# Performance work log

Hardware: AMD Instinct MI355X
Metric: run time of the kernel (lower is better)

Reference implementation:

```python
import jax, jax.numpy as jnp
import numpy as np

B, C_IN, T = 32, 192, 8192
H, N_PH, OUT = 192, 1024, 4
EPS = 1e-5


def setup_inputs() -> dict:
    key = jax.random.key(0)
    ks = jax.random.split(key, 12)
    s = 0.02
    return {
        "x": jax.random.normal(ks[0], (B, C_IN, T), jnp.float32),
        "x_mask": jnp.ones((B, 1, N_PH), jnp.float32),
        "w": jax.random.randint(ks[1], (B, 1, N_PH), 0, 8, jnp.int32),
        "pre_w": jax.random.normal(ks[2], (H, C_IN), jnp.float32) * s,
        "pre_b": jnp.zeros((H,), jnp.float32),
        "conv0_w": jax.random.normal(ks[3], (H, H, 3), jnp.float32) * s,
        "conv0_b": jnp.zeros((H,), jnp.float32),
        "ln0_g": jnp.ones((H,), jnp.float32),
        "ln0_b": jnp.zeros((H,), jnp.float32),
        "conv1_w": jax.random.normal(ks[4], (H, H, 3), jnp.float32) * s,
        "conv1_b": jnp.zeros((H,), jnp.float32),
        "ln1_g": jnp.ones((H,), jnp.float32),
        "ln1_b": jnp.zeros((H,), jnp.float32),
        "lin_w": jax.random.normal(ks[5], (OUT, H), jnp.float32) * s,
        "lin_b": jnp.zeros((OUT,), jnp.float32),
    }


def _segment_mean(x, w2):
    # x: [B, C, T] frames; w2: [B, n_ph] int durations.
    # Faithful to the torch double loop: phoneme j pools frames
    # [cumsum(w)[j-1] : cumsum(w)[j]); w==0 -> zeros.
    ends = jnp.cumsum(w2, axis=1)                      # [B, n_ph]
    t = jnp.arange(x.shape[2], dtype=ends.dtype)       # [T]
    ph_id = jax.vmap(lambda e: jnp.searchsorted(e, t, side="right"))(ends)  # [B, T]
    # segment sums over frames; extra segment n_ph catches out-of-range frames
    sums = jax.vmap(lambda xt, ids: jax.ops.segment_sum(xt, ids, num_segments=N_PH + 1))(
        x.transpose(0, 2, 1), ph_id
    )                                                  # [B, n_ph+1, C]
    sums = sums[:, :N_PH].transpose(0, 2, 1)           # [B, C, n_ph]
    denom = jnp.maximum(w2, 1).astype(x.dtype)[:, None, :]
    return jnp.where(w2[:, None, :] > 0, sums / denom, 0.0)


def _conv3(x, k, b):
    y = jax.lax.conv_general_dilated(x, k, (1,), [(1, 1)],
                                     dimension_numbers=("NCH", "OIH", "NCH"))
    return y + b[None, :, None]


def _ln(x, g, b):
    # channel-dim LayerNorm for [B, C, T] (VITS modules.LayerNorm)
    m = jnp.mean(x, axis=1, keepdims=True)
    v = jnp.mean(jnp.square(x - m), axis=1, keepdims=True)
    return (x - m) * jax.lax.rsqrt(v + EPS) * g[None, :, None] + b[None, :, None]


def reference(x, x_mask, w, pre_w, pre_b, conv0_w, conv0_b, ln0_g, ln0_b,
              conv1_w, conv1_b, ln1_g, ln1_b, lin_w, lin_b):
    w2 = w.reshape(w.shape[0], -1).astype(jnp.int32)
    spec = _segment_mean(x, w2)                                 # [B, C_in, n_ph]
    h = jnp.einsum("bct,hc->bht", spec, pre_w) + pre_b[None, :, None]
    # block 0: conv -> relu -> LN (dropout is identity at eval), mask before each layer
    h = _conv3(h * x_mask, conv0_w, conv0_b)
    h = jax.nn.relu(h * x_mask)
    h = _ln(h * x_mask, ln0_g, ln0_b)
    h = h * x_mask  # dropout(p=0.1) at eval = identity; mask still applied
    # block 1
    h = _conv3(h * x_mask, conv1_w, conv1_b)
    h = jax.nn.relu(h * x_mask)
    h = _ln(h * x_mask, ln1_g, ln1_b)
    h = h * x_mask
    p = jnp.einsum("bht,oh->bot", h, lin_w) + lin_b[None, :, None]
    return p * x_mask
```

## Files before the change

kernel.cpp:

```cpp
#include <hip/hip_runtime.h>
#include <hip/hip_bf16.h>

#define B 32
#define C_IN 192
#define T 8192
#define H 192
#define N_PH 1024
#define OUT 4
#define PROWS (N_PH + 2)
#define ROWP (2 * H)

typedef __attribute__((ext_vector_type(8))) short short8;
typedef __attribute__((ext_vector_type(4))) float f32x4;
typedef unsigned short ushort_t;

__device__ inline ushort_t f2bf(float f) {
    unsigned u = __builtin_bit_cast(unsigned, f);
    unsigned r = u + 0x7fffu + ((u >> 16) & 1u);
    return (ushort_t)(r >> 16);
}
__device__ inline float bf2f(ushort_t h) {
    unsigned u = ((unsigned)h) << 16;
    return __builtin_bit_cast(float, u);
}
__device__ inline void split_bf(float x, ushort_t& hi, ushort_t& lo) {
    hi = f2bf(x);
    lo = f2bf(x - bf2f(hi));
}

__device__ inline void wfrag_one(const float* __restrict__ w, ushort_t* __restrict__ wtf,
                                 int taps, int idx, int ntot) {
    int j  = idx & 7;
    int l  = (idx >> 3) & 63;
    int slot = idx >> 9;
    int nt = slot % 12;
    int ss = (slot / 12) % 6;
    int kt = slot / 72;
    int o  = nt * 16 + (l & 15);
    int i  = ss * 32 + ((l >> 4) << 3) + j;
    float v = (taps == 1) ? w[o * C_IN + i] : w[(o * H + i) * 3 + kt];
    ushort_t hi, lo;
    split_bf(v, hi, lo);
    wtf[idx] = hi;
    wtf[idx + ntot] = lo;
}

#define NWF 1008
__global__ __launch_bounds__(256) void prep_kernel(
    const float* __restrict__ pw, const float* __restrict__ w0,
    const float* __restrict__ w1, const int* __restrict__ wdur,
    ushort_t* __restrict__ wpre, ushort_t* __restrict__ w0t,
    ushort_t* __restrict__ w1t, int* __restrict__ ends)
{
    int blk = blockIdx.x;
    int tid = threadIdx.x;
    const int n1 = 36864, n3 = 110592;
    if (blk < NWF) {
        int idx = blk * 256 + tid;
        if (idx < n1) { wfrag_one(pw, wpre, 1, idx, n1); return; }
        idx -= n1;
        if (idx < n3) { wfrag_one(w0, w0t, 3, idx, n3); return; }
        idx -= n3;
        if (idx < n3) wfrag_one(w1, w1t, 3, idx, n3);
        return;
    }
    int b = blk - NWF;
    __shared__ int part[256];
    int4 w4 = ((const int4*)(wdur + b * N_PH))[tid];
    int c0 = w4.x, c1 = c0 + w4.y, c2 = c1 + w4.z, c3 = c2 + w4.w;
    part[tid] = c3;
    __syncthreads();
    for (int off = 1; off < 256; off <<= 1) {
        int v = (tid >= off) ? part[tid - off] : 0;
        __syncthreads();
        part[tid] += v;
        __syncthreads();
    }
    int pre = tid ? part[tid - 1] : 0;
    int4 e4;
    e4.x = pre + c0; e4.y = pre + c1; e4.z = pre + c2; e4.w = pre + c3;
    ((int4*)(ends + b * N_PH))[tid] = e4;
}

__global__ __launch_bounds__(256) void segmean_direct_kernel(
    const float* __restrict__ x, const int* __restrict__ ends,
    ushort_t* __restrict__ specT)
{
    int b  = blockIdx.x >> 5;
    int jt = (blockIdx.x & 31) * 32;
    int tid = threadIdx.x;
    int j_loc = tid & 31;
    int cg0 = tid >> 5;
    int j = jt + j_loc;

    __shared__ float sm[32][193];

    const int* eb = ends + b * N_PH;
    int e0 = eb[j];
    int s0 = j ? eb[j - 1] : 0;
    int len = e0 - s0;
    float inv = (len > 0) ? 1.f / (float)len : 0.f;

    const float* xb = x + (size_t)b * C_IN * T;
#pragma unroll 1
    for (int c = cg0; c < C_IN; c += 8) {
        const float* xr = xb + (size_t)c * T;
        float sum = 0.f;
        for (int t = s0; t < e0; ++t) sum += xr[t];
        sm[j_loc][c] = sum * inv;
    }
    __syncthreads();

    int r = tid >> 3;
    int g = tid & 7;
    ushort_t* ob = specT + ((size_t)b * N_PH + jt + r) * ROWP;
#pragma unroll
    for (int i0 = 0; i0 < 24; i0 += 8) {
        ushort_t th[8], tl[8];
#pragma unroll
        for (int k2 = 0; k2 < 8; ++k2) {
            int c = g * 24 + i0 + k2;
            split_bf(sm[r][c], th[k2], tl[k2]);
        }
        *(short8*)(ob + g * 24 + i0) = *(short8*)th;
        *(short8*)(ob + H + g * 24 + i0) = *(short8*)tl;
    }
}

#define LOADOPS(IT, AH0, AL0, AH1, AL1, BH, BL) do {                              \
    int kt_ = (IT) / 6, s_ = (IT) - kt_ * 6;                                      \
    const ushort_t* arow_ = inb + (long)(trow + kt_ - pad) * ROWP + s_ * 32 + kg; \
    AH0 = *(const short8*)(arow_);                                                \
    AL0 = *(const short8*)(arow_ + H);                                            \
    AH1 = *(const short8*)(arow_ + 16 * ROWP);                                    \
    AL1 = *(const short8*)(arow_ + 16 * ROWP + H);                                \
    const ushort_t* wb_ = wt + ((size_t)((kt_ * 6 + s_) * 12 + nhalf * 6) << 9)   \
                        + (lane << 3);                                            \
    _Pragma("unroll") for (int n_ = 0; n_ < 6; ++n_) {                            \
        BH[n_] = *(const short8*)(wb_ + (n_ << 9));                               \
        BL[n_] = *(const short8*)(wb_ + (n_ << 9) + ntotw); }                     \
} while (0)

#define DOMFMA(AH0, AL0, AH1, AL1, BH, BL) do {                                             \
    _Pragma("unroll") for (int n_ = 0; n_ < 6; ++n_) {                                      \
        acc[0][n_] = __builtin_amdgcn_mfma_f32_16x16x32_bf16(AH0, BH[n_], acc[0][n_], 0,0,0); \
        acc[0][n_] = __builtin_amdgcn_mfma_f32_16x16x32_bf16(AL0, BH[n_], acc[0][n_], 0,0,0); \
        acc[0][n_] = __builtin_amdgcn_mfma_f32_16x16x32_bf16(AH0, BL[n_], acc[0][n_], 0,0,0); \
        acc[1][n_] = __builtin_amdgcn_mfma_f32_16x16x32_bf16(AH1, BH[n_], acc[1][n_], 0,0,0); \
        acc[1][n_] = __builtin_amdgcn_mfma_f32_16x16x32_bf16(AL1, BH[n_], acc[1][n_], 0,0,0); \
        acc[1][n_] = __builtin_amdgcn_mfma_f32_16x16x32_bf16(AH1, BL[n_], acc[1][n_], 0,0,0); } \
} while (0)

__global__ __launch_bounds__(256) void gemm_fused_kernel(
    const ushort_t* __restrict__ in, int in_rows,
    const ushort_t* __restrict__ wt,
    const float* __restrict__ bias,
    const float* __restrict__ mask,
    const float* __restrict__ g, const float* __restrict__ beta,
    ushort_t* __restrict__ out,
    const float* __restrict__ lw, const float* __restrict__ lb,
    float* __restrict__ fout,
    int taps, int do_ln, int nmask, int fin)
{
    int b  = blockIdx.y;
    int t0 = blockIdx.x * 64;
    int tid = threadIdx.x;
    int lane = tid & 63;
    int wv = tid >> 6;
    int mhalf = wv & 1;
    int nhalf = wv >> 1;

    __shared__ float ep[64][193];
    __shared__ float g_s[H], b_s[H], m_s[64], mstat[64], rstat[64];
    if (tid < H) { g_s[tid] = do_ln ? g[tid] : 1.f; b_s[tid] = do_ln ? beta[tid] : 0.f; }
    if (tid < 64) m_s[tid] = mask[b * N_PH + t0 + tid];

    short8 z8 = {0, 0, 0, 0, 0, 0, 0, 0};
    if (!fin) {
        if (t0 == 0 && tid < ROWP / 8)
            *(short8*)(out + (size_t)b * PROWS * ROWP + tid * 8) = z8;
        if (t0 == N_PH - 64 && tid < ROWP / 8)
            *(short8*)(out + ((size_t)b * PROWS + N_PH + 1) * ROWP + tid * 8) = z8;
    }

    int m  = lane & 15;
    int kg = (lane >> 4) << 3;
    int ntotw = taps * 36864;
    int pad = taps >> 1;

    const ushort_t* inb = in + (size_t)b * in_rows * ROWP;
    int trow = t0 + mhalf * 32 + m;

    f32x4 acc[2][6];
#pragma unroll
    for (int ntl = 0; ntl < 6; ++ntl) {
        float bb = bias[(nhalf * 6 + ntl) * 16 + m];
        acc[0][ntl] = (f32x4){bb, bb, bb, bb};
        acc[1][ntl] = (f32x4){bb, bb, bb, bb};
    }

    short8 pah0, pal0, pah1, pal1, pbh[6], pbl[6];
    short8 qah0, qal0, qah1, qal1, qbh[6], qbl[6];
    int iters = taps * 6;
    LOADOPS(0, pah0, pal0, pah1, pal1, pbh, pbl);
#pragma unroll 1
    for (int it = 0; it < iters; it += 2) {
        LOADOPS(it + 1, qah0, qal0, qah1, qal1, qbh, qbl);
        DOMFMA(pah0, pal0, pah1, pal1, pbh, pbl);
        if (it + 2 < iters) LOADOPS(it + 2, pah0, pal0, pah1, pal1, pbh, pbl);
        DOMFMA(qah0, qal0, qah1, qal1, qbh, qbl);
    }

    __syncthreads();

    int rbase = (lane >> 4) << 2;
#pragma unroll
    for (int mh = 0; mh < 2; ++mh) {
#pragma unroll
        for (int ntl = 0; ntl < 6; ++ntl) {
            int o = (nhalf * 6 + ntl) * 16 + m;
#pragma unroll
            for (int r = 0; r < 4; ++r) {
                int t_loc = mhalf * 32 + mh * 16 + rbase + r;
                float mm = m_s[t_loc];
                float v = acc[mh][ntl][r];
                if (do_ln) {
                    v = fmaxf(v * mm, 0.f) * mm;
                } else {
                    for (int q = 0; q < nmask; ++q) v *= mm;
                }
                ep[t_loc][o] = v;
            }
        }
    }
    __syncthreads();

    if (do_ln && tid < 64) {
        float s = 0.f, ss = 0.f;
        for (int c = 0; c < H; ++c) {
            float v = ep[tid][c];
            s += v;
            ss += v * v;
        }
        float mean = s * (1.f / (float)H);
        mstat[tid] = mean;
        rstat[tid] = rsqrtf(ss * (1.f / (float)H) - mean * mean + 1e-5f);
    }
    __syncthreads();

    int row = tid >> 2;
    int q = tid & 3;
    if (fin) {
        float mean = mstat[row], rstd = rstat[row], mk = m_s[row];
        float a0 = 0.f, a1 = 0.f, a2 = 0.f, a3 = 0.f;
#pragma unroll 1
        for (int c = q * 48; c < q * 48 + 48; ++c) {
            float y = ((ep[row][c] - mean) * rstd * g_s[c] + b_s[c]) * mk;
            a0 += lw[0 * H + c] * y;
            a1 += lw[1 * H + c] * y;
            a2 += lw[2 * H + c] * y;
            a3 += lw[3 * H + c] * y;
        }
        a0 += __shfl_xor(a0, 1); a0 += __shfl_xor(a0, 2);
        a1 += __shfl_xor(a1, 1); a1 += __shfl_xor(a1, 2);
        a2 += __shfl_xor(a2, 1); a2 += __shfl_xor(a2, 2);
        a3 += __shfl_xor(a3, 1); a3 += __shfl_xor(a3, 2);
        if (q == 0) {
            int t = t0 + row;
            float* ob = fout + (size_t)b * OUT * N_PH + t;
            ob[0 * N_PH] = (a0 + lb[0]) * mk;
            ob[1 * N_PH] = (a1 + lb[1]) * mk;
            ob[2 * N_PH] = (a2 + lb[2]) * mk;
            ob[3 * N_PH] = (a3 + lb[3]) * mk;
        }
        return;
    }

    float mean = 0.f, rstd = 1.f, mfac = 1.f;
    if (do_ln) {
        mean = mstat[row];
        rstd = rstat[row];
        float mk = m_s[row];
        mfac = (nmask == 2) ? mk * mk : mk;
    }
    ushort_t* orow = out + ((size_t)b * PROWS + t0 + row + 1) * ROWP + q * 48;
#pragma unroll
    for (int i0 = 0; i0 < 48; i0 += 8) {
        ushort_t th[8], tl[8];
#pragma unroll
        for (int k2 = 0; k2 < 8; ++k2) {
            int c = q * 48 + i0 + k2;
            float v = ep[row][c];
            float y = do_ln ? ((v - mean) * rstd * g_s[c] + b_s[c]) * mfac : v;
            split_bf(y, th[k2], tl[k2]);
        }
        *(short8*)(orow + i0) = *(short8*)th;
        *(short8*)(orow + H + i0) = *(short8*)tl;
    }
}

extern "C" void kernel_launch(void* const* d_in, const int* in_sizes, int n_in,
                              void* d_out, int out_size, void* d_ws, size_t ws_size,
                              hipStream_t stream) {
    const float* x      = (const float*)d_in[0];
    const float* x_mask = (const float*)d_in[1];
    const int*   w      = (const int*)d_in[2];
    const float* pre_w  = (const float*)d_in[3];
    const float* pre_b  = (const float*)d_in[4];
    const float* conv0_w = (const float*)d_in[5];
    const float* conv0_b = (const float*)d_in[6];
    const float* ln0_g   = (const float*)d_in[7];
    const float* ln0_b   = (const float*)d_in[8];
    const float* conv1_w = (const float*)d_in[9];
    const float* conv1_b = (const float*)d_in[10];
    const float* ln1_g   = (const float*)d_in[11];
    const float* ln1_b   = (const float*)d_in[12];
    const float* lin_w   = (const float*)d_in[13];
    const float* lin_b   = (const float*)d_in[14];
    float* out = (float*)d_out;

    char* ws = (char*)d_ws;
    size_t off = 0;
    ushort_t* bufA = (ushort_t*)(ws + off); off += (size_t)B * PROWS * ROWP * sizeof(ushort_t);
    ushort_t* bufB = (ushort_t*)(ws + off); off += (size_t)B * PROWS * ROWP * sizeof(ushort_t);
    ushort_t* wpre = (ushort_t*)(ws + off); off += (size_t)2 * 36864 * sizeof(ushort_t);
    ushort_t* w0t  = (ushort_t*)(ws + off); off += (size_t)2 * 110592 * sizeof(ushort_t);
    ushort_t* w1t  = (ushort_t*)(ws + off); off += (size_t)2 * 110592 * sizeof(ushort_t);
    int* ends      = (int*)(ws + off);      off += (size_t)B * N_PH * sizeof(int);
    ushort_t* specT = bufB;

    prep_kernel<<<NWF + B, 256, 0, stream>>>(pre_w, conv0_w, conv1_w, w,
                                             wpre, w0t, w1t, ends);

    segmean_direct_kernel<<<B * 32, 256, 0, stream>>>(x, ends, specT);

    dim3 gg(N_PH / 64, B);
    gemm_fused_kernel<<<gg, 256, 0, stream>>>(specT, N_PH, wpre, pre_b, x_mask,
                                              ln0_g, ln0_b, bufA,
                                              nullptr, nullptr, nullptr, 1, 0, 1, 0);
    gemm_fused_kernel<<<gg, 256, 0, stream>>>(bufA + ROWP, PROWS, w0t, conv0_b, x_mask,
                                              ln0_g, ln0_b, bufB,
                                              nullptr, nullptr, nullptr, 3, 1, 2, 0);
    gemm_fused_kernel<<<gg, 256, 0, stream>>>(bufB + ROWP, PROWS, w1t, conv1_b, x_mask,
                                              ln1_g, ln1_b, bufA,
                                              lin_w, lin_b, out, 3, 1, 1, 1);
}
```

Before: 401.8 us.

## Fuse pre-projection, both conv blocks and output linear into one halo-tiled kernel

```diff
diff --git a/kernel.cpp b/kernel.cpp
--- a/kernel.cpp
+++ b/kernel.cpp
@@ -7,8 +7,8 @@
 #define H 192
 #define N_PH 1024
 #define OUT 4
-#define PROWS (N_PH + 2)
 #define ROWP (2 * H)
+#define HPITCH 392
 
 typedef __attribute__((ext_vector_type(8))) short short8;
 typedef __attribute__((ext_vector_type(4))) float f32x4;
@@ -127,139 +127,273 @@
     }
 }
 
-#define LOADOPS(IT, AH0, AL0, AH1, AL1, BH, BL) do {                              \
-    int kt_ = (IT) / 6, s_ = (IT) - kt_ * 6;                                      \
-    const ushort_t* arow_ = inb + (long)(trow + kt_ - pad) * ROWP + s_ * 32 + kg; \
-    AH0 = *(const short8*)(arow_);                                                \
-    AL0 = *(const short8*)(arow_ + H);                                            \
-    AH1 = *(const short8*)(arow_ + 16 * ROWP);                                    \
-    AL1 = *(const short8*)(arow_ + 16 * ROWP + H);                                \
-    const ushort_t* wb_ = wt + ((size_t)((kt_ * 6 + s_) * 12 + nhalf * 6) << 9)   \
-                        + (lane << 3);                                            \
-    _Pragma("unroll") for (int n_ = 0; n_ < 6; ++n_) {                            \
-        BH[n_] = *(const short8*)(wb_ + (n_ << 9));                               \
-        BL[n_] = *(const short8*)(wb_ + (n_ << 9) + ntotw); }                     \
-} while (0)
-
-#define DOMFMA(AH0, AL0, AH1, AL1, BH, BL) do {                                             \
-    _Pragma("unroll") for (int n_ = 0; n_ < 6; ++n_) {                                      \
-        acc[0][n_] = __builtin_amdgcn_mfma_f32_16x16x32_bf16(AH0, BH[n_], acc[0][n_], 0,0,0); \
-        acc[0][n_] = __builtin_amdgcn_mfma_f32_16x16x32_bf16(AL0, BH[n_], acc[0][n_], 0,0,0); \
-        acc[0][n_] = __builtin_amdgcn_mfma_f32_16x16x32_bf16(AH0, BL[n_], acc[0][n_], 0,0,0); \
-        acc[1][n_] = __builtin_amdgcn_mfma_f32_16x16x32_bf16(AH1, BH[n_], acc[1][n_], 0,0,0); \
-        acc[1][n_] = __builtin_amdgcn_mfma_f32_16x16x32_bf16(AL1, BH[n_], acc[1][n_], 0,0,0); \
-        acc[1][n_] = __builtin_amdgcn_mfma_f32_16x16x32_bf16(AH1, BL[n_], acc[1][n_], 0,0,0); } \
-} while (0)
-
-__global__ __launch_bounds__(256) void gemm_fused_kernel(
-    const ushort_t* __restrict__ in, int in_rows,
-    const ushort_t* __restrict__ wt,
-    const float* __restrict__ bias,
+__global__ __launch_bounds__(256) void chain_kernel(
+    const ushort_t* __restrict__ specT,
+    const ushort_t* __restrict__ wpre, const ushort_t* __restrict__ w0t,
+    const ushort_t* __restrict__ w1t,
+    const float* __restrict__ pre_b, const float* __restrict__ c0_b,
+    const float* __restrict__ c1_b,
     const float* __restrict__ mask,
-    const float* __restrict__ g, const float* __restrict__ beta,
-    ushort_t* __restrict__ out,
+    const float* __restrict__ g0, const float* __restrict__ be0,
+    const float* __restrict__ g1, const float* __restrict__ be1,
     const float* __restrict__ lw, const float* __restrict__ lb,
-    float* __restrict__ fout,
-    int taps, int do_ln, int nmask, int fin)
+    float* __restrict__ out)
 {
-    int b  = blockIdx.y;
-    int t0 = blockIdx.x * 64;
-    int tid = threadIdx.x;
-    int lane = tid & 63;
-    int wv = tid >> 6;
-    int mhalf = wv & 1;
-    int nhalf = wv >> 1;
-
-    __shared__ float ep[64][193];
-    __shared__ float g_s[H], b_s[H], m_s[64], mstat[64], rstat[64];
-    if (tid < H) { g_s[tid] = do_ln ? g[tid] : 1.f; b_s[tid] = do_ln ? beta[tid] : 0.f; }
-    if (tid < 64) m_s[tid] = mask[b * N_PH + t0 + tid];
-
-    short8 z8 = {0, 0, 0, 0, 0, 0, 0, 0};
-    if (!fin) {
-        if (t0 == 0 && tid < ROWP / 8)
-            *(short8*)(out + (size_t)b * PROWS * ROWP + tid * 8) = z8;
-        if (t0 == N_PH - 64 && tid < ROWP / 8)
-            *(short8*)(out + ((size_t)b * PROWS + N_PH + 1) * ROWP + tid * 8) = z8;
-    }
-
-    int m  = lane & 15;
-    int kg = (lane >> 4) << 3;
-    int ntotw = taps * 36864;
-    int pad = taps >> 1;
-
-    const ushort_t* inb = in + (size_t)b * in_rows * ROWP;
-    int trow = t0 + mhalf * 32 + m;
-
-    f32x4 acc[2][6];
-#pragma unroll
-    for (int ntl = 0; ntl < 6; ++ntl) {
-        float bb = bias[(nhalf * 6 + ntl) * 16 + m];
-        acc[0][ntl] = (f32x4){bb, bb, bb, bb};
-        acc[1][ntl] = (f32x4){bb, bb, bb, bb};
-    }
-
-    short8 pah0, pal0, pah1, pal1, pbh[6], pbl[6];
-    short8 qah0, qal0, qah1, qal1, qbh[6], qbl[6];
-    int iters = taps * 6;
-    LOADOPS(0, pah0, pal0, pah1, pal1, pbh, pbl);
-#pragma unroll 1
-    for (int it = 0; it < iters; it += 2) {
-        LOADOPS(it + 1, qah0, qal0, qah1, qal1, qbh, qbl);
-        DOMFMA(pah0, pal0, pah1, pal1, pbh, pbl);
-        if (it + 2 < iters) LOADOPS(it + 2, pah0, pal0, pah1, pal1, pbh, pbl);
-        DOMFMA(qah0, qal0, qah1, qal1, qbh, qbl);
-    }
-
-    __syncthreads();
-
-    int rbase = (lane >> 4) << 2;
-#pragma unroll
-    for (int mh = 0; mh < 2; ++mh) {
-#pragma unroll
-        for (int ntl = 0; ntl < 6; ++ntl) {
-            int o = (nhalf * 6 + ntl) * 16 + m;
-#pragma unroll
-            for (int r = 0; r < 4; ++r) {
-                int t_loc = mhalf * 32 + mh * 16 + rbase + r;
-                float mm = m_s[t_loc];
-                float v = acc[mh][ntl][r];
-                if (do_ln) {
-                    v = fmaxf(v * mm, 0.f) * mm;
-                } else {
-                    for (int q = 0; q < nmask; ++q) v *= mm;
-                }
-                ep[t_loc][o] = v;
-            }
-        }
-    }
-    __syncthreads();
-
-    if (do_ln && tid < 64) {
+    const int b  = blockIdx.y;
+    const int t0 = blockIdx.x * 64;
+    const int tid = threadIdx.x;
+    const int lane = tid & 63;
+    const int wv = tid >> 6;
+    const int nhalf = wv >> 1;
+    const int mgrp = wv & 1;
+    const int m = lane & 15;
+    const int kg = (lane >> 4) << 3;
+    const int rbase = (lane >> 4) << 2;
+
+    __shared__ ushort_t hbuf[82 * HPITCH];
+    __shared__ float g0_s[H], b0_s[H], g1_s[H], b1_s[H];
+    __shared__ float lw_s[OUT * H];
+    __shared__ float m_s[96], mstat[66], rstat[66];
+
+    if (tid < H) { g0_s[tid] = g0[tid]; b0_s[tid] = be0[tid];
+                   g1_s[tid] = g1[tid]; b1_s[tid] = be1[tid]; }
+    if (tid < 96) {
+        int grow = t0 - 2 + tid;
+        m_s[tid] = (grow >= 0 && grow < N_PH) ? mask[b * N_PH + grow] : 0.f;
+    }
+    for (int i = tid; i < OUT * H; i += 256) lw_s[i] = lw[i];
+    __syncthreads();
+
+    const short8 z8 = {0, 0, 0, 0, 0, 0, 0, 0};
+
+    {
+        f32x4 acc[3][6];
+#pragma unroll
+        for (int n = 0; n < 6; ++n) {
+            float bb = pre_b[(nhalf * 6 + n) * 16 + m];
+#pragma unroll
+            for (int f = 0; f < 3; ++f) acc[f][n] = (f32x4){bb, bb, bb, bb};
+        }
+        const ushort_t* inb = specT + (size_t)b * N_PH * ROWP;
+#pragma unroll 1
+        for (int s = 0; s < 6; ++s) {
+            short8 ah[3], al[3], bh[6], bl[6];
+#pragma unroll
+            for (int f = 0; f < 3; ++f) {
+                int trow = t0 - 2 + (mgrp * 3 + f) * 16 + m;
+                if ((unsigned)trow < (unsigned)N_PH) {
+                    const ushort_t* ar = inb + (size_t)trow * ROWP + s * 32 + kg;
+                    ah[f] = *(const short8*)ar;
+                    al[f] = *(const short8*)(ar + H);
+                } else { ah[f] = z8; al[f] = z8; }
+            }
+            const ushort_t* wb = wpre + ((size_t)(s * 12 + nhalf * 6) << 9) + (lane << 3);
+#pragma unroll
+            for (int n = 0; n < 6; ++n) {
+                bh[n] = *(const short8*)(wb + (n << 9));
+                bl[n] = *(const short8*)(wb + (n << 9) + 36864);
+            }
+#pragma unroll
+            for (int f = 0; f < 3; ++f)
+#pragma unroll
+                for (int n = 0; n < 6; ++n) {
+                    acc[f][n] = __builtin_amdgcn_mfma_f32_16x16x32_bf16(ah[f], bh[n], acc[f][n], 0, 0, 0);
+                    acc[f][n] = __builtin_amdgcn_mfma_f32_16x16x32_bf16(al[f], bh[n], acc[f][n], 0, 0, 0);
+                    acc[f][n] = __builtin_amdgcn_mfma_f32_16x16x32_bf16(ah[f], bl[n], acc[f][n], 0, 0, 0);
+                }
+        }
+#pragma unroll
+        for (int f = 0; f < 3; ++f) {
+            int lb0 = (mgrp * 3 + f) * 16 + rbase;
+#pragma unroll
+            for (int n = 0; n < 6; ++n) {
+                int col = (nhalf * 6 + n) * 16 + m;
+#pragma unroll
+                for (int r = 0; r < 4; ++r) {
+                    int l = lb0 + r;
+                    if (l < 82) {
+                        float v = acc[f][n][r] * m_s[l];
+                        ushort_t hi, lo; split_bf(v, hi, lo);
+                        hbuf[l * HPITCH + col] = hi;
+                        hbuf[l * HPITCH + H + col] = lo;
+                    }
+                }
+            }
+        }
+    }
+    __syncthreads();
+
+    {
+        f32x4 acc[3][6];
+        const int nf = mgrp ? 2 : 3;
+        const int fbase = mgrp * 3;
+#pragma unroll
+        for (int n = 0; n < 6; ++n) {
+            float bb = c0_b[(nhalf * 6 + n) * 16 + m];
+#pragma unroll
+            for (int f = 0; f < 3; ++f) acc[f][n] = (f32x4){bb, bb, bb, bb};
+        }
+#pragma unroll 1
+        for (int kt = 0; kt < 3; ++kt)
+#pragma unroll 1
+            for (int s = 0; s < 6; ++s) {
+                short8 ah[3], al[3], bh[6], bl[6];
+#pragma unroll
+                for (int f = 0; f < 3; ++f) {
+                    if (f < nf) {
+                        int l0 = (fbase + f) * 16 + m + kt;
+                        const ushort_t* ar = hbuf + l0 * HPITCH + s * 32 + kg;
+                        ah[f] = *(const short8*)ar;
+                        al[f] = *(const short8*)(ar + H);
+                    }
+                }
+                const ushort_t* wb = w0t + ((size_t)((kt * 6 + s) * 12 + nhalf * 6) << 9) + (lane << 3);
+#pragma unroll
+                for (int n = 0; n < 6; ++n) {
+                    bh[n] = *(const short8*)(wb + (n << 9));
+                    bl[n] = *(const short8*)(wb + (n << 9) + 110592);
+                }
+#pragma unroll
+                for (int f = 0; f < 3; ++f) {
+                    if (f < nf) {
+#pragma unroll
+                        for (int n = 0; n < 6; ++n) {
+                            acc[f][n] = __builtin_amdgcn_mfma_f32_16x16x32_bf16(ah[f], bh[n], acc[f][n], 0, 0, 0);
+                            acc[f][n] = __builtin_amdgcn_mfma_f32_16x16x32_bf16(al[f], bh[n], acc[f][n], 0, 0, 0);
+                            acc[f][n] = __builtin_amdgcn_mfma_f32_16x16x32_bf16(ah[f], bl[n], acc[f][n], 0, 0, 0);
+                        }
+                    }
+                }
+            }
+        __syncthreads();
+#pragma unroll
+        for (int f = 0; f < 3; ++f) {
+            if (f < nf) {
+                int lb1 = (fbase + f) * 16 + rbase;
+#pragma unroll
+                for (int n = 0; n < 6; ++n) {
+                    int col = (nhalf * 6 + n) * 16 + m;
+#pragma unroll
+                    for (int r = 0; r < 4; ++r) {
+                        int l = lb1 + r;
+                        if (l < 66) {
+                            float mm = m_s[l + 1];
+                            float u = fmaxf(acc[f][n][r] * mm, 0.f) * mm;
+                            ushort_t hi, lo; split_bf(u, hi, lo);
+                            hbuf[l * HPITCH + col] = hi;
+                            hbuf[l * HPITCH + H + col] = lo;
+                        }
+                    }
+                }
+            }
+        }
+    }
+    __syncthreads();
+
+    if (tid < 66) {
         float s = 0.f, ss = 0.f;
         for (int c = 0; c < H; ++c) {
-            float v = ep[tid][c];
-            s += v;
-            ss += v * v;
+            float v = bf2f(hbuf[tid * HPITCH + c]) + bf2f(hbuf[tid * HPITCH + H + c]);
+            s += v; ss += v * v;
         }
         float mean = s * (1.f / (float)H);
         mstat[tid] = mean;
         rstat[tid] = rsqrtf(ss * (1.f / (float)H) - mean * mean + 1e-5f);
     }
     __syncthreads();
-
-    int row = tid >> 2;
-    int q = tid & 3;
-    if (fin) {
-        float mean = mstat[row], rstd = rstat[row], mk = m_s[row];
+    for (int idx = tid; idx < 66 * H; idx += 256) {
+        int row = idx / H;
+        int c = idx - row * H;
+        float v = bf2f(hbuf[row * HPITCH + c]) + bf2f(hbuf[row * HPITCH + H + c]);
+        float mm = m_s[row + 1];
+        float y = ((v - mstat[row]) * rstat[row] * g0_s[c] + b0_s[c]) * (mm * mm);
+        ushort_t hi, lo; split_bf(y, hi, lo);
+        hbuf[row * HPITCH + c] = hi;
+        hbuf[row * HPITCH + H + c] = lo;
+    }
+    __syncthreads();
+
+    {
+        f32x4 acc[2][6];
+#pragma unroll
+        for (int n = 0; n < 6; ++n) {
+            float bb = c1_b[(nhalf * 6 + n) * 16 + m];
+            acc[0][n] = (f32x4){bb, bb, bb, bb};
+            acc[1][n] = (f32x4){bb, bb, bb, bb};
+        }
+#pragma unroll 1
+        for (int kt = 0; kt < 3; ++kt)
+#pragma unroll 1
+            for (int s = 0; s < 6; ++s) {
+                short8 ah[2], al[2], bh[6], bl[6];
+#pragma unroll
+                for (int f = 0; f < 2; ++f) {
+                    int l1 = (mgrp * 2 + f) * 16 + m + kt;
+                    const ushort_t* ar = hbuf + l1 * HPITCH + s * 32 + kg;
+                    ah[f] = *(const short8*)ar;
+                    al[f] = *(const short8*)(ar + H);
+                }
+                const ushort_t* wb = w1t + ((size_t)((kt * 6 + s) * 12 + nhalf * 6) << 9) + (lane << 3);
+#pragma unroll
+                for (int n = 0; n < 6; ++n) {
+                    bh[n] = *(const short8*)(wb + (n << 9));
+                    bl[n] = *(const short8*)(wb + (n << 9) + 110592);
+                }
+#pragma unroll
+                for (int f = 0; f < 2; ++f)
+#pragma unroll
+                    for (int n = 0; n < 6; ++n) {
+                        acc[f][n] = __builtin_amdgcn_mfma_f32_16x16x32_bf16(ah[f], bh[n], acc[f][n], 0, 0, 0);
+                        acc[f][n] = __builtin_amdgcn_mfma_f32_16x16x32_bf16(al[f], bh[n], acc[f][n], 0, 0, 0);
+                        acc[f][n] = __builtin_amdgcn_mfma_f32_16x16x32_bf16(ah[f], bl[n], acc[f][n], 0, 0, 0);
+                    }
+            }
+        __syncthreads();
+#pragma unroll
+        for (int f = 0; f < 2; ++f) {
+            int lb2 = (mgrp * 2 + f) * 16 + rbase;
+#pragma unroll
+            for (int n = 0; n < 6; ++n) {
+                int col = (nhalf * 6 + n) * 16 + m;
+#pragma unroll
+                for (int r = 0; r < 4; ++r) {
+                    int l = lb2 + r;
+                    float mm = m_s[l + 2];
+                    float u = fmaxf(acc[f][n][r] * mm, 0.f) * mm;
+                    ushort_t hi, lo; split_bf(u, hi, lo);
+                    hbuf[l * HPITCH + col] = hi;
+                    hbuf[l * HPITCH + H + col] = lo;
+                }
+            }
+        }
+    }
+    __syncthreads();
+
+    if (tid < 64) {
+        float s = 0.f, ss = 0.f;
+        for (int c = 0; c < H; ++c) {
+            float v = bf2f(hbuf[tid * HPITCH + c]) + bf2f(hbuf[tid * HPITCH + H + c]);
+            s += v; ss += v * v;
+        }
+        float mean = s * (1.f / (float)H);
+        mstat[tid] = mean;
+        rstat[tid] = rsqrtf(ss * (1.f / (float)H) - mean * mean + 1e-5f);
+    }
+    __syncthreads();
+
+    {
+        int row = tid >> 2;
+        int q = tid & 3;
+        float mean = mstat[row], rstd = rstat[row], mk = m_s[row + 2];
         float a0 = 0.f, a1 = 0.f, a2 = 0.f, a3 = 0.f;
 #pragma unroll 1
         for (int c = q * 48; c < q * 48 + 48; ++c) {
-            float y = ((ep[row][c] - mean) * rstd * g_s[c] + b_s[c]) * mk;
-            a0 += lw[0 * H + c] * y;
-            a1 += lw[1 * H + c] * y;
-            a2 += lw[2 * H + c] * y;
-            a3 += lw[3 * H + c] * y;
+            float v = bf2f(hbuf[row * HPITCH + c]) + bf2f(hbuf[row * HPITCH + H + c]);
+            float y = ((v - mean) * rstd * g1_s[c] + b1_s[c]) * mk;
+            a0 += lw_s[0 * H + c] * y;
+            a1 += lw_s[1 * H + c] * y;
+            a2 += lw_s[2 * H + c] * y;
+            a3 += lw_s[3 * H + c] * y;
         }
         a0 += __shfl_xor(a0, 1); a0 += __shfl_xor(a0, 2);
         a1 += __shfl_xor(a1, 1); a1 += __shfl_xor(a1, 2);
@@ -267,35 +401,12 @@
         a3 += __shfl_xor(a3, 1); a3 += __shfl_xor(a3, 2);
         if (q == 0) {
             int t = t0 + row;
-            float* ob = fout + (size_t)b * OUT * N_PH + t;
+            float* ob = out + (size_t)b * OUT * N_PH + t;
             ob[0 * N_PH] = (a0 + lb[0]) * mk;
             ob[1 * N_PH] = (a1 + lb[1]) * mk;
             ob[2 * N_PH] = (a2 + lb[2]) * mk;
             ob[3 * N_PH] = (a3 + lb[3]) * mk;
         }
-        return;
-    }
-
-    float mean = 0.f, rstd = 1.f, mfac = 1.f;
-    if (do_ln) {
-        mean = mstat[row];
-        rstd = rstat[row];
-        float mk = m_s[row];
-        mfac = (nmask == 2) ? mk * mk : mk;
-    }
-    ushort_t* orow = out + ((size_t)b * PROWS + t0 + row + 1) * ROWP + q * 48;
-#pragma unroll
-    for (int i0 = 0; i0 < 48; i0 += 8) {
-        ushort_t th[8], tl[8];
-#pragma unroll
-        for (int k2 = 0; k2 < 8; ++k2) {
-            int c = q * 48 + i0 + k2;
-            float v = ep[row][c];
-            float y = do_ln ? ((v - mean) * rstd * g_s[c] + b_s[c]) * mfac : v;
-            split_bf(y, th[k2], tl[k2]);
-        }
-        *(short8*)(orow + i0) = *(short8*)th;
-        *(short8*)(orow + H + i0) = *(short8*)tl;
     }
 }
 
@@ -321,27 +432,18 @@
 
     char* ws = (char*)d_ws;
     size_t off = 0;
-    ushort_t* bufA = (ushort_t*)(ws + off); off += (size_t)B * PROWS * ROWP * sizeof(ushort_t);
-    ushort_t* bufB = (ushort_t*)(ws + off); off += (size_t)B * PROWS * ROWP * sizeof(ushort_t);
-    ushort_t* wpre = (ushort_t*)(ws + off); off += (size_t)2 * 36864 * sizeof(ushort_t);
-    ushort_t* w0t  = (ushort_t*)(ws + off); off += (size_t)2 * 110592 * sizeof(ushort_t);
-    ushort_t* w1t  = (ushort_t*)(ws + off); off += (size_t)2 * 110592 * sizeof(ushort_t);
-    int* ends      = (int*)(ws + off);      off += (size_t)B * N_PH * sizeof(int);
-    ushort_t* specT = bufB;
+    ushort_t* specT = (ushort_t*)(ws + off); off += (size_t)B * N_PH * ROWP * sizeof(ushort_t);
+    ushort_t* wpre  = (ushort_t*)(ws + off); off += (size_t)2 * 36864 * sizeof(ushort_t);
+    ushort_t* w0t   = (ushort_t*)(ws + off); off += (size_t)2 * 110592 * sizeof(ushort_t);
+    ushort_t* w1t   = (ushort_t*)(ws + off); off += (size_t)2 * 110592 * sizeof(ushort_t);
+    int* ends       = (int*)(ws + off);      off += (size_t)B * N_PH * sizeof(int);
 
     prep_kernel<<<NWF + B, 256, 0, stream>>>(pre_w, conv0_w, conv1_w, w,
                                              wpre, w0t, w1t, ends);
 
     segmean_direct_kernel<<<B * 32, 256, 0, stream>>>(x, ends, specT);
 
-    dim3 gg(N_PH / 64, B);
-    gemm_fused_kernel<<<gg, 256, 0, stream>>>(specT, N_PH, wpre, pre_b, x_mask,
-                                              ln0_g, ln0_b, bufA,
-                                              nullptr, nullptr, nullptr, 1, 0, 1, 0);
-    gemm_fused_kernel<<<gg, 256, 0, stream>>>(bufA + ROWP, PROWS, w0t, conv0_b, x_mask,
-                                              ln0_g, ln0_b, bufB,
-                                              nullptr, nullptr, nullptr, 3, 1, 2, 0);
-    gemm_fused_kernel<<<gg, 256, 0, stream>>>(bufB + ROWP, PROWS, w1t, conv1_b, x_mask,
-                                              ln1_g, ln1_b, bufA,
-                                              lin_w, lin_b, out, 3, 1, 1, 1);
-}
+    chain_kernel<<<dim3(N_PH / 64, B), 256, 0, stream>>>(
+        specT, wpre, w0t, w1t, pre_b, conv0_b, conv1_b, x_mask,
+        ln0_g, ln0_b, ln1_g, ln1_b, lin_w, lin_b, out);
+}
```

New measurement: 376.6 us. -6.3%, faster.
